# Performance work log

Hardware: AMD Instinct MI355X
Metric: run time of the kernel (lower is better)

Reference implementation:

```python
import jax, jax.numpy as jnp
import numpy as np

D_ENC, D_PRED, D_JOINT, VOCAB = 512, 640, 640, 1024
LOGIT_CLAMP = 15.0


def setup_inputs() -> dict:
    key = jax.random.key(0)
    ks = jax.random.split(key, 8)
    B, T, U = 4, 256, 64
    enc = jax.random.normal(ks[0], (B, T, D_ENC), dtype=jnp.float32)
    pred = jax.random.normal(ks[1], (B, U, D_PRED), dtype=jnp.float32)
    s_e = 1.0 / np.sqrt(D_ENC)
    s_p = 1.0 / np.sqrt(D_PRED)
    s_j = 1.0 / np.sqrt(D_JOINT)
    W_enc = jax.random.uniform(ks[2], (D_ENC, D_JOINT), jnp.float32, -s_e, s_e)
    b_enc = jax.random.uniform(ks[3], (D_JOINT,), jnp.float32, -s_e, s_e)
    W_pred = jax.random.uniform(ks[4], (D_PRED, D_JOINT), jnp.float32, -s_p, s_p)
    b_pred = jax.random.uniform(ks[5], (D_JOINT,), jnp.float32, -s_p, s_p)
    W_out = jax.random.uniform(ks[6], (D_JOINT, VOCAB), jnp.float32, -s_j, s_j)
    b_out = jax.random.uniform(ks[7], (VOCAB,), jnp.float32, -s_j, s_j)
    return {"encoder_out": enc, "predictor_out": pred,
            "W_enc": W_enc, "b_enc": b_enc,
            "W_pred": W_pred, "b_pred": b_pred,
            "W_out": W_out, "b_out": b_out}


def reference(encoder_out, predictor_out, W_enc, b_enc, W_pred, b_pred, W_out, b_out):
    # (B,T,d_joint) and (B,U,d_joint) projections
    enc = jnp.einsum('bte,ej->btj', encoder_out, W_enc) + b_enc
    pred = jnp.einsum('bup,pj->buj', predictor_out, W_pred) + b_pred
    # broadcast add -> (B,T,U,d_joint), tanh, vocab projection
    joint = jnp.tanh(enc[:, :, None, :] + pred[:, None, :, :])
    logits = jnp.einsum('btuj,jv->btuv', joint, W_out) + b_out
    return jnp.clip(logits, -LOGIT_CLAMP, LOGIT_CLAMP)
```

## Files before the change

### kernel.cpp

```cpp
#include <hip/hip_runtime.h>

typedef unsigned short u16;
typedef unsigned int u32;
typedef __bf16 bf16x8 __attribute__((ext_vector_type(8)));
typedef float f32x4 __attribute__((ext_vector_type(4)));

#define T_DIM 256
#define U_DIM 64
#define DJ 640
#define VOCAB 1024

typedef __attribute__((address_space(3))) u32 lds_u32;
typedef const __attribute__((address_space(1))) u32 glb_u32;

__device__ __forceinline__ u16 f2bf(float f) {
    u32 x = __float_as_uint(f);
    x += 0x7fffu + ((x >> 16) & 1u);
    return (u16)(x >> 16);
}

__device__ __forceinline__ float fast_tanh(float x) {
    float e = __expf(2.0f * x);
    return 1.0f - 2.0f / (e + 1.0f);
}

__global__ __launch_bounds__(256) void convert_wout(const float* __restrict__ W,
                                                    u16* __restrict__ Wt) {
    __shared__ float tile[32][33];
    int tx = threadIdx.x & 31, ty = threadIdx.x >> 5;
    int n0 = blockIdx.x * 32, k0 = blockIdx.y * 32;
#pragma unroll
    for (int j = 0; j < 4; j++)
        tile[ty + j * 8][tx] = W[(size_t)(k0 + ty + j * 8) * VOCAB + n0 + tx];
    __syncthreads();
#pragma unroll
    for (int j = 0; j < 4; j++)
        Wt[(size_t)(n0 + ty + j * 8) * DJ + k0 + tx] = f2bf(tile[tx][ty + j * 8]);
}

template <int K>
__global__ __launch_bounds__(128) void proj_kernel(const float* __restrict__ X,
                                                   const float* __restrict__ W,
                                                   const float* __restrict__ bias,
                                                   float* __restrict__ out) {
    __shared__ float xs[4][K];
    int r0 = blockIdx.x * 4;
    int jj = blockIdx.y * 128 + threadIdx.x;
    for (int idx = threadIdx.x; idx < 4 * K; idx += 128) {
        int r = idx / K, k = idx - r * K;
        xs[r][k] = X[(size_t)(r0 + r) * K + k];
    }
    __syncthreads();
    float b = bias[jj];
    float a0 = b, a1 = b, a2 = b, a3 = b;
#pragma unroll 8
    for (int k = 0; k < K; k++) {
        float w = W[(size_t)k * DJ + jj];
        a0 = fmaf(xs[0][k], w, a0);
        a1 = fmaf(xs[1][k], w, a1);
        a2 = fmaf(xs[2][k], w, a2);
        a3 = fmaf(xs[3][k], w, a3);
    }
    out[(size_t)(r0 + 0) * DJ + jj] = a0;
    out[(size_t)(r0 + 1) * DJ + jj] = a1;
    out[(size_t)(r0 + 2) * DJ + jj] = a2;
    out[(size_t)(r0 + 3) * DJ + jj] = a3;
}

__global__ __launch_bounds__(256) void tanh_kernel(const float* __restrict__ encp,
                                                   const float* __restrict__ predp,
                                                   u16* __restrict__ A) {
    int id = blockIdx.x * 256 + threadIdx.x;
    int m = id / 80;
    int c = id - m * 80;
    int koff = c * 8;
    int b = m >> 14, t = (m >> 6) & 255, u = m & 63;
    const float4* pe = (const float4*)(encp + (size_t)(b * T_DIM + t) * DJ + koff);
    const float4* pp = (const float4*)(predp + (size_t)(b * U_DIM + u) * DJ + koff);
    float4 e0 = pe[0], e1 = pe[1];
    float4 p0 = pp[0], p1 = pp[1];
    uint4 v;
    v.x = (u32)f2bf(fast_tanh(e0.x + p0.x)) | ((u32)f2bf(fast_tanh(e0.y + p0.y)) << 16);
    v.y = (u32)f2bf(fast_tanh(e0.z + p0.z)) | ((u32)f2bf(fast_tanh(e0.w + p0.w)) << 16);
    v.z = (u32)f2bf(fast_tanh(e1.x + p1.x)) | ((u32)f2bf(fast_tanh(e1.y + p1.y)) << 16);
    v.w = (u32)f2bf(fast_tanh(e1.z + p1.z)) | ((u32)f2bf(fast_tanh(e1.w + p1.w)) << 16);
    *(uint4*)(A + (size_t)id * 8) = v;
}

__global__ __launch_bounds__(256) void gemm_kernel(const u16* __restrict__ A,
                                                   const u16* __restrict__ Wt,
                                                   const float* __restrict__ b_out,
                                                   float* __restrict__ out) {
    __shared__ u16 As[128 * 64];
    __shared__ u16 Bs[128 * 64];

    int bid = blockIdx.x;
    int swz = (bid & 7) * 512 + (bid >> 3);
    int ntile = swz & 7;
    int mtile = swz >> 3;
    int row0 = mtile * 128;
    int n0 = ntile * 128;

    int tid = threadIdx.x;
    int lane = tid & 63;
    int wave = tid >> 6;
    int wm = wave & 1;
    int wn = wave >> 1;
    int lm = lane & 15;
    int quad = lane >> 4;

    int rS = wave * 8 + (lane >> 3);
    int kSwz = ((lane ^ (lane >> 3)) & 7) * 8;
    const u16* gA = A + (size_t)(row0 + rS) * DJ + kSwz;
    const u16* gB = Wt + (size_t)(n0 + rS) * DJ + kSwz;
    u16* lA = As + wave * 8 * 64;
    u16* lB = Bs + wave * 8 * 64;

    int abase = (wm * 64 + lm) * 64;
    int bbase = (wn * 64 + lm) * 64;
    int c0 = ((quad ^ (lm & 7))) * 8;
    int c1 = (((quad ^ 4) ^ (lm & 7))) * 8;

    f32x4 acc[4][4];
#pragma unroll
    for (int i = 0; i < 4; i++)
#pragma unroll
        for (int j = 0; j < 4; j++) {
            acc[i][j][0] = 0.f; acc[i][j][1] = 0.f;
            acc[i][j][2] = 0.f; acc[i][j][3] = 0.f;
        }

    for (int k0 = 0; k0 < DJ; k0 += 64) {
#pragma unroll
        for (int i = 0; i < 4; i++) {
            __builtin_amdgcn_global_load_lds((glb_u32*)(gA + (size_t)i * 32 * DJ + k0),
                                             (lds_u32*)(lA + i * 32 * 64), 16, 0, 0);
            __builtin_amdgcn_global_load_lds((glb_u32*)(gB + (size_t)i * 32 * DJ + k0),
                                             (lds_u32*)(lB + i * 32 * 64), 16, 0, 0);
        }
        __syncthreads();

        bf16x8 af[4], bfr[4];
#pragma unroll
        for (int i = 0; i < 4; i++)
            af[i] = *(const bf16x8*)(As + abase + i * 16 * 64 + c0);
#pragma unroll
        for (int j = 0; j < 4; j++)
            bfr[j] = *(const bf16x8*)(Bs + bbase + j * 16 * 64 + c0);
#pragma unroll
        for (int i = 0; i < 4; i++)
#pragma unroll
            for (int j = 0; j < 4; j++)
                acc[i][j] = __builtin_amdgcn_mfma_f32_16x16x32_bf16(af[i], bfr[j], acc[i][j], 0, 0, 0);
#pragma unroll
        for (int i = 0; i < 4; i++)
            af[i] = *(const bf16x8*)(As + abase + i * 16 * 64 + c1);
#pragma unroll
        for (int j = 0; j < 4; j++)
            bfr[j] = *(const bf16x8*)(Bs + bbase + j * 16 * 64 + c1);
#pragma unroll
        for (int i = 0; i < 4; i++)
#pragma unroll
            for (int j = 0; j < 4; j++)
                acc[i][j] = __builtin_amdgcn_mfma_f32_16x16x32_bf16(af[i], bfr[j], acc[i][j], 0, 0, 0);

        __syncthreads();
    }

#pragma unroll
    for (int j = 0; j < 4; j++) {
        int gc = n0 + wn * 64 + j * 16 + lm;
        float bo = b_out[gc];
#pragma unroll
        for (int i = 0; i < 4; i++) {
            int gr = row0 + wm * 64 + i * 16 + quad * 4;
#pragma unroll
            for (int r = 0; r < 4; r++) {
                float v = acc[i][j][r] + bo;
                v = fminf(fmaxf(v, -15.0f), 15.0f);
                out[(size_t)(gr + r) * VOCAB + gc] = v;
            }
        }
    }
}

#define LDA 40
__global__ __launch_bounds__(256) void joint_fused(const float* __restrict__ encp,
                                                   const float* __restrict__ predp,
                                                   const u16* __restrict__ Wt,
                                                   const float* __restrict__ b_out,
                                                   float* __restrict__ out) {
    __shared__ u16 As[128 * LDA];
    __shared__ u16 Bs[128 * LDA];
    int ntile = blockIdx.x & 7;
    int mtile = blockIdx.x >> 3;
    int row0 = mtile * 128;
    int bidx = row0 >> 14;
    int t0 = (row0 & 16383) >> 6;
    int n0 = ntile * 128;
    int tid = threadIdx.x, lane = tid & 63, wave = tid >> 6;
    int wm = wave & 1, wn = wave >> 1, lm = lane & 15, quad = lane >> 4;
    int am = tid >> 1, ak = (tid & 1) << 4;
    const float* encA = encp + (size_t)(bidx * T_DIM + t0 + (am >> 6)) * DJ + ak;
    const float* predA = predp + (size_t)(bidx * U_DIM + (am & 63)) * DJ + ak;
    u16* Asw = As + am * LDA + ak;
    int bn = tid >> 1, bk = (tid & 1) << 4;
    const u16* WtB = Wt + (size_t)(n0 + bn) * DJ + bk;
    u16* Bsw = Bs + bn * LDA + bk;
    f32x4 acc[4][4];
#pragma unroll
    for (int i = 0; i < 4; i++)
#pragma unroll
        for (int j = 0; j < 4; j++) {
            acc[i][j][0] = 0.f; acc[i][j][1] = 0.f; acc[i][j][2] = 0.f; acc[i][j][3] = 0.f;
        }
    for (int k0 = 0; k0 < DJ; k0 += 32) {
        const float4* pe = (const float4*)(encA + k0);
        const float4* pp = (const float4*)(predA + k0);
#pragma unroll
        for (int i = 0; i < 4; i++) {
            float4 e = pe[i]; float4 p = pp[i];
            uint2 v;
            v.x = (u32)f2bf(fast_tanh(e.x + p.x)) | ((u32)f2bf(fast_tanh(e.y + p.y)) << 16);
            v.y = (u32)f2bf(fast_tanh(e.z + p.z)) | ((u32)f2bf(fast_tanh(e.w + p.w)) << 16);
            *(uint2*)(Asw + i * 4) = v;
        }
        const u16* src = WtB + k0;
        uint4 w0 = *(const uint4*)src;
        uint4 w1 = *(const uint4*)(src + 8);
        *(uint4*)Bsw = w0;
        *(uint4*)(Bsw + 8) = w1;
        __syncthreads();
        bf16x8 af[4], bfr[4];
#pragma unroll
        for (int i = 0; i < 4; i++)
            af[i] = *(const bf16x8*)(As + (wm * 64 + i * 16 + lm) * LDA + quad * 8);
#pragma unroll
        for (int j = 0; j < 4; j++)
            bfr[j] = *(const bf16x8*)(Bs + (wn * 64 + j * 16 + lm) * LDA + quad * 8);
#pragma unroll
        for (int i = 0; i < 4; i++)
#pragma unroll
            for (int j = 0; j < 4; j++)
                acc[i][j] = __builtin_amdgcn_mfma_f32_16x16x32_bf16(af[i], bfr[j], acc[i][j], 0, 0, 0);
        __syncthreads();
    }
#pragma unroll
    for (int j = 0; j < 4; j++) {
        int gc = n0 + wn * 64 + j * 16 + lm;
        float bo = b_out[gc];
#pragma unroll
        for (int i = 0; i < 4; i++) {
            int gr = row0 + wm * 64 + i * 16 + quad * 4;
#pragma unroll
            for (int r = 0; r < 4; r++) {
                float v = acc[i][j][r] + bo;
                v = fminf(fmaxf(v, -15.0f), 15.0f);
                out[(size_t)(gr + r) * VOCAB + gc] = v;
            }
        }
    }
}

extern "C" void kernel_launch(void* const* d_in, const int* in_sizes, int n_in,
                              void* d_out, int out_size, void* d_ws, size_t ws_size,
                              hipStream_t stream) {
    const float* enc    = (const float*)d_in[0];
    const float* pred   = (const float*)d_in[1];
    const float* W_enc  = (const float*)d_in[2];
    const float* b_enc  = (const float*)d_in[3];
    const float* W_pred = (const float*)d_in[4];
    const float* b_pred = (const float*)d_in[5];
    const float* W_out  = (const float*)d_in[6];
    const float* b_out  = (const float*)d_in[7];
    float* out = (float*)d_out;

    float* enc_proj  = (float*)d_ws;
    float* pred_proj = enc_proj + 1024 * DJ;
    u16*   Wt        = (u16*)(pred_proj + 256 * DJ);
    u16*   Abuf      = Wt + 1024 * DJ;

    size_t need = (size_t)(1024 + 256) * DJ * 4 + (size_t)1024 * DJ * 2
                + (size_t)65536 * DJ * 2;

    convert_wout<<<dim3(32, 20), dim3(256), 0, stream>>>(W_out, Wt);
    proj_kernel<512><<<dim3(256, 5), dim3(128), 0, stream>>>(enc, W_enc, b_enc, enc_proj);
    proj_kernel<640><<<dim3(64, 5), dim3(128), 0, stream>>>(pred, W_pred, b_pred, pred_proj);

    if (ws_size >= need) {
        tanh_kernel<<<dim3(65536 * 80 / 256), dim3(256), 0, stream>>>(enc_proj, pred_proj, Abuf);
        gemm_kernel<<<dim3(4096), dim3(256), 0, stream>>>(Abuf, Wt, b_out, out);
    } else {
        joint_fused<<<dim3(4096), dim3(256), 0, stream>>>(enc_proj, pred_proj, Wt, b_out, out);
    }
}
```

Before: 516.5 us.

## Fuse tanh broadcast-add into swizzled GEMM A-tile loading

Drops the separate tanh kernel that wrote a 65536x640 bf16 intermediate buffer. The GEMM now builds each A tile in LDS by computing tanh(enc+pred) from the fp32 projections, keeping the existing XOR swizzle and the async global-to-LDS loads for the weights. This removes the round trip of roughly 84MB through HBM plus one launch. The cost is that tanh is recomputed once per N tile (8 times per element), and synchronous fp32 loads and ALU work now sit in the GEMM main loop.

```diff
diff --git a/kernel.cpp b/kernel.cpp
--- a/kernel.cpp
+++ b/kernel.cpp
@@ -67,30 +67,11 @@
     out[(size_t)(r0 + 3) * DJ + jj] = a3;
 }
 
-__global__ __launch_bounds__(256) void tanh_kernel(const float* __restrict__ encp,
-                                                   const float* __restrict__ predp,
-                                                   u16* __restrict__ A) {
-    int id = blockIdx.x * 256 + threadIdx.x;
-    int m = id / 80;
-    int c = id - m * 80;
-    int koff = c * 8;
-    int b = m >> 14, t = (m >> 6) & 255, u = m & 63;
-    const float4* pe = (const float4*)(encp + (size_t)(b * T_DIM + t) * DJ + koff);
-    const float4* pp = (const float4*)(predp + (size_t)(b * U_DIM + u) * DJ + koff);
-    float4 e0 = pe[0], e1 = pe[1];
-    float4 p0 = pp[0], p1 = pp[1];
-    uint4 v;
-    v.x = (u32)f2bf(fast_tanh(e0.x + p0.x)) | ((u32)f2bf(fast_tanh(e0.y + p0.y)) << 16);
-    v.y = (u32)f2bf(fast_tanh(e0.z + p0.z)) | ((u32)f2bf(fast_tanh(e0.w + p0.w)) << 16);
-    v.z = (u32)f2bf(fast_tanh(e1.x + p1.x)) | ((u32)f2bf(fast_tanh(e1.y + p1.y)) << 16);
-    v.w = (u32)f2bf(fast_tanh(e1.z + p1.z)) | ((u32)f2bf(fast_tanh(e1.w + p1.w)) << 16);
-    *(uint4*)(A + (size_t)id * 8) = v;
-}
-
-__global__ __launch_bounds__(256) void gemm_kernel(const u16* __restrict__ A,
-                                                   const u16* __restrict__ Wt,
-                                                   const float* __restrict__ b_out,
-                                                   float* __restrict__ out) {
+__global__ __launch_bounds__(256) void fused_gemm(const float* __restrict__ encp,
+                                                  const float* __restrict__ predp,
+                                                  const u16* __restrict__ Wt,
+                                                  const float* __restrict__ b_out,
+                                                  float* __restrict__ out) {
     __shared__ u16 As[128 * 64];
     __shared__ u16 Bs[128 * 64];
 
@@ -111,10 +92,11 @@
 
     int rS = wave * 8 + (lane >> 3);
     int kSwz = ((lane ^ (lane >> 3)) & 7) * 8;
-    const u16* gA = A + (size_t)(row0 + rS) * DJ + kSwz;
     const u16* gB = Wt + (size_t)(n0 + rS) * DJ + kSwz;
-    u16* lA = As + wave * 8 * 64;
     u16* lB = Bs + wave * 8 * 64;
+
+    int bt0 = row0 >> 6;
+    int bu0 = (row0 >> 14) * 64;
 
     int abase = (wm * 64 + lm) * 64;
     int bbase = (wn * 64 + lm) * 64;
@@ -132,11 +114,26 @@
 
     for (int k0 = 0; k0 < DJ; k0 += 64) {
 #pragma unroll
-        for (int i = 0; i < 4; i++) {
-            __builtin_amdgcn_global_load_lds((glb_u32*)(gA + (size_t)i * 32 * DJ + k0),
-                                             (lds_u32*)(lA + i * 32 * 64), 16, 0, 0);
+        for (int i = 0; i < 4; i++)
             __builtin_amdgcn_global_load_lds((glb_u32*)(gB + (size_t)i * 32 * DJ + k0),
                                              (lds_u32*)(lB + i * 32 * 64), 16, 0, 0);
+
+#pragma unroll
+        for (int j = 0; j < 4; j++) {
+            int ch = tid + j * 256;
+            int r = ch >> 3;
+            int c = ch & 7;
+            int k8 = k0 + c * 8;
+            const float4* pe = (const float4*)(encp + (size_t)(bt0 + (r >> 6)) * DJ + k8);
+            const float4* pp = (const float4*)(predp + (size_t)(bu0 + (r & 63)) * DJ + k8);
+            float4 e0 = pe[0], e1 = pe[1];
+            float4 p0 = pp[0], p1 = pp[1];
+            uint4 v;
+            v.x = (u32)f2bf(fast_tanh(e0.x + p0.x)) | ((u32)f2bf(fast_tanh(e0.y + p0.y)) << 16);
+            v.y = (u32)f2bf(fast_tanh(e0.z + p0.z)) | ((u32)f2bf(fast_tanh(e0.w + p0.w)) << 16);
+            v.z = (u32)f2bf(fast_tanh(e1.x + p1.x)) | ((u32)f2bf(fast_tanh(e1.y + p1.y)) << 16);
+            v.w = (u32)f2bf(fast_tanh(e1.z + p1.z)) | ((u32)f2bf(fast_tanh(e1.w + p1.w)) << 16);
+            *(uint4*)(As + r * 64 + ((c ^ (r & 7)) * 8)) = v;
         }
         __syncthreads();
 
@@ -167,84 +164,6 @@
         __syncthreads();
     }
 
-#pragma unroll
-    for (int j = 0; j < 4; j++) {
-        int gc = n0 + wn * 64 + j * 16 + lm;
-        float bo = b_out[gc];
-#pragma unroll
-        for (int i = 0; i < 4; i++) {
-            int gr = row0 + wm * 64 + i * 16 + quad * 4;
-#pragma unroll
-            for (int r = 0; r < 4; r++) {
-                float v = acc[i][j][r] + bo;
-                v = fminf(fmaxf(v, -15.0f), 15.0f);
-                out[(size_t)(gr + r) * VOCAB + gc] = v;
-            }
-        }
-    }
-}
-
-#define LDA 40
-__global__ __launch_bounds__(256) void joint_fused(const float* __restrict__ encp,
-                                                   const float* __restrict__ predp,
-                                                   const u16* __restrict__ Wt,
-                                                   const float* __restrict__ b_out,
-                                                   float* __restrict__ out) {
-    __shared__ u16 As[128 * LDA];
-    __shared__ u16 Bs[128 * LDA];
-    int ntile = blockIdx.x & 7;
-    int mtile = blockIdx.x >> 3;
-    int row0 = mtile * 128;
-    int bidx = row0 >> 14;
-    int t0 = (row0 & 16383) >> 6;
-    int n0 = ntile * 128;
-    int tid = threadIdx.x, lane = tid & 63, wave = tid >> 6;
-    int wm = wave & 1, wn = wave >> 1, lm = lane & 15, quad = lane >> 4;
-    int am = tid >> 1, ak = (tid & 1) << 4;
-    const float* encA = encp + (size_t)(bidx * T_DIM + t0 + (am >> 6)) * DJ + ak;
-    const float* predA = predp + (size_t)(bidx * U_DIM + (am & 63)) * DJ + ak;
-    u16* Asw = As + am * LDA + ak;
-    int bn = tid >> 1, bk = (tid & 1) << 4;
-    const u16* WtB = Wt + (size_t)(n0 + bn) * DJ + bk;
-    u16* Bsw = Bs + bn * LDA + bk;
-    f32x4 acc[4][4];
-#pragma unroll
-    for (int i = 0; i < 4; i++)
-#pragma unroll
-        for (int j = 0; j < 4; j++) {
-            acc[i][j][0] = 0.f; acc[i][j][1] = 0.f; acc[i][j][2] = 0.f; acc[i][j][3] = 0.f;
-        }
-    for (int k0 = 0; k0 < DJ; k0 += 32) {
-        const float4* pe = (const float4*)(encA + k0);
-        const float4* pp = (const float4*)(predA + k0);
-#pragma unroll
-        for (int i = 0; i < 4; i++) {
-            float4 e = pe[i]; float4 p = pp[i];
-            uint2 v;
-            v.x = (u32)f2bf(fast_tanh(e.x + p.x)) | ((u32)f2bf(fast_tanh(e.y + p.y)) << 16);
-            v.y = (u32)f2bf(fast_tanh(e.z + p.z)) | ((u32)f2bf(fast_tanh(e.w + p.w)) << 16);
-            *(uint2*)(Asw + i * 4) = v;
-        }
-        const u16* src = WtB + k0;
-        uint4 w0 = *(const uint4*)src;
-        uint4 w1 = *(const uint4*)(src + 8);
-        *(uint4*)Bsw = w0;
-        *(uint4*)(Bsw + 8) = w1;
-        __syncthreads();
-        bf16x8 af[4], bfr[4];
-#pragma unroll
-        for (int i = 0; i < 4; i++)
-            af[i] = *(const bf16x8*)(As + (wm * 64 + i * 16 + lm) * LDA + quad * 8);
-#pragma unroll
-        for (int j = 0; j < 4; j++)
-            bfr[j] = *(const bf16x8*)(Bs + (wn * 64 + j * 16 + lm) * LDA + quad * 8);
-#pragma unroll
-        for (int i = 0; i < 4; i++)
-#pragma unroll
-            for (int j = 0; j < 4; j++)
-                acc[i][j] = __builtin_amdgcn_mfma_f32_16x16x32_bf16(af[i], bfr[j], acc[i][j], 0, 0, 0);
-        __syncthreads();
-    }
 #pragma unroll
     for (int j = 0; j < 4; j++) {
         int gc = n0 + wn * 64 + j * 16 + lm;
@@ -278,19 +197,9 @@
     float* enc_proj  = (float*)d_ws;
     float* pred_proj = enc_proj + 1024 * DJ;
     u16*   Wt        = (u16*)(pred_proj + 256 * DJ);
-    u16*   Abuf      = Wt + 1024 * DJ;
-
-    size_t need = (size_t)(1024 + 256) * DJ * 4 + (size_t)1024 * DJ * 2
-                + (size_t)65536 * DJ * 2;
 
     convert_wout<<<dim3(32, 20), dim3(256), 0, stream>>>(W_out, Wt);
     proj_kernel<512><<<dim3(256, 5), dim3(128), 0, stream>>>(enc, W_enc, b_enc, enc_proj);
     proj_kernel<640><<<dim3(64, 5), dim3(128), 0, stream>>>(pred, W_pred, b_pred, pred_proj);
-
-    if (ws_size >= need) {
-        tanh_kernel<<<dim3(65536 * 80 / 256), dim3(256), 0, stream>>>(enc_proj, pred_proj, Abuf);
-        gemm_kernel<<<dim3(4096), dim3(256), 0, stream>>>(Abuf, Wt, b_out, out);
-    } else {
-        joint_fused<<<dim3(4096), dim3(256), 0, stream>>>(enc_proj, pred_proj, Wt, b_out, out);
-    }
-}
+    fused_gemm<<<dim3(4096), dim3(256), 0, stream>>>(enc_proj, pred_proj, Wt, b_out, out);
+}
```

Measured after the change: 595.5 us. 15.3% more time.
